# Kernel tuning notes

Measured on AMD Instinct MI355X. Metric: run time of the kernel, lower is better.

## Reference

```python
import jax, jax.numpy as jnp
import numpy as np

MARGIN = 0.3
NEG_FALLBACK = 1e6  # value used when a row has no negatives


def setup_inputs() -> dict:
    key = jax.random.key(0)
    k1, k2 = jax.random.split(key)
    N, D, NUM_IDS = 8192, 256, 512
    feat = jax.random.normal(k1, (N, D), dtype=jnp.float32)
    labels = jax.random.randint(k2, (N,), 0, NUM_IDS, dtype=jnp.int64)
    return {"feat": feat, "labels": labels}


def reference(feat, labels):
    N = feat.shape[0]
    sq_norms = jnp.sum(feat * feat, axis=1)  # [N]
    sq = sq_norms[:, None] + sq_norms[None, :] - 2.0 * (feat @ feat.T)  # [N,N]
    sq = jnp.maximum(sq, 0.0)
    # safe sqrt (zero distance on the diagonal would otherwise give nan grads)
    dist = jnp.where(sq > 0, jnp.sqrt(jnp.where(sq > 0, sq, 1.0)), 0.0)

    same = labels[:, None] == labels[None, :]          # [N,N] bool
    eye = jnp.eye(N, dtype=bool)
    is_pos = same & ~eye                                # exclude self-pair
    is_neg = ~same

    # hard mining: per-row masked max over positives / min over negatives
    dist_ap = jnp.where(is_pos.any(axis=1),
                        jnp.where(is_pos, dist, -jnp.inf).max(axis=1), 0.0)
    dist_an = jnp.where(is_neg.any(axis=1),
                        jnp.where(is_neg, dist, jnp.inf).min(axis=1), NEG_FALLBACK)

    # MarginRankingLoss with y=1: mean(relu(margin - (dist_an - dist_ap)))
    return jnp.mean(jnp.maximum(0.0, MARGIN + dist_ap - dist_an))
```

## Files before the change

### kernel.cpp

```cpp
#include <hip/hip_runtime.h>


constexpr int N = 8192;
constexpr int D = 256;
constexpr float MARGIN = 0.3f;
constexpr float NEG_FALLBACK = 1e6f;
constexpr float TBIG = 1e30f;

typedef __attribute__((ext_vector_type(8))) __bf16 bf16x8;
typedef __attribute__((ext_vector_type(4))) float f32x4;

__device__ __forceinline__ unsigned enc_f(float f) {
  unsigned u = __float_as_uint(f);
  return (u >> 31) ? ~u : (u | 0x80000000u);
}
__device__ __forceinline__ float dec_f(unsigned e) {
  unsigned u = (e >> 31) ? (e ^ 0x80000000u) : ~e;
  return __uint_as_float(u);
}
__device__ __forceinline__ unsigned short f2bf_rtn(float x) {
  unsigned u = __float_as_uint(x);
  return (unsigned short)((u + 0x7fffu + ((u >> 16) & 1u)) >> 16);
}


__global__ void tl_pass0f(const float* __restrict__ feat, float* __restrict__ norms,
                          unsigned* __restrict__ ap, unsigned* __restrict__ an,
                          unsigned short* __restrict__ P, float* __restrict__ out) {
  int row = blockIdx.x * 4 + (threadIdx.x >> 6);
  int lane = threadIdx.x & 63;
  float4 f = reinterpret_cast<const float4*>(feat + (size_t)row * D)[lane];
  ushort4 h;
  h.x = f2bf_rtn(f.x); h.y = f2bf_rtn(f.y); h.z = f2bf_rtn(f.z); h.w = f2bf_rtn(f.w);
  reinterpret_cast<ushort4*>(P + (size_t)row * D)[lane] = h;
  float s = fmaf(f.x, f.x, fmaf(f.y, f.y, fmaf(f.z, f.z, f.w * f.w)));
#pragma unroll
  for (int off = 32; off > 0; off >>= 1) s += __shfl_down(s, off, 64);
  if (lane == 0) {
    norms[row] = s;
    ap[row] = enc_f(-TBIG);
    an[row] = enc_f(TBIG);
  }
  if (row == 0 && lane == 0) out[0] = 0.0f;
}


__global__ __launch_bounds__(256, 3)
void tl_pass1m(const unsigned short* __restrict__ P, const int* __restrict__ labels,
               const float* __restrict__ norms,
               unsigned* __restrict__ ap, unsigned* __restrict__ an) {
  __shared__ unsigned short lbuf[2][128][64];

  unsigned short (*lA)[64] = lbuf[0];
  unsigned short (*lB)[64] = lbuf[1];

  const int tid = threadIdx.x;
  const int wave = tid >> 6;
  const int lane = tid & 63;
  const int c = lane & 15;
  const int q = lane >> 4;
  const int ib0 = blockIdx.y * 128;
  const int jb0 = blockIdx.x * 128;
  const int wi = (wave & 1) * 64;
  const int wj = (wave >> 1) * 64;

  f32x4 acc[4][4];
#pragma unroll
  for (int a = 0; a < 4; ++a)
#pragma unroll
    for (int b = 0; b < 4; ++b) acc[a][b] = (f32x4){0.f, 0.f, 0.f, 0.f};

  const int rsub = lane >> 3;
  const int gsw = (lane & 7) ^ (rsub & 7);

  for (int kc = 0; kc < D; kc += 64) {
#pragma unroll
    for (int t = 0; t < 4; ++t) {
      int rA = wave * 32 + t * 8;
      const unsigned short* gA = P + (size_t)(ib0 + rA + rsub) * D + kc + gsw * 8;
      __builtin_amdgcn_global_load_lds(
          (const __attribute__((address_space(1))) void*)gA,
          (__attribute__((address_space(3))) void*)&lA[rA][0], 16, 0, 0);
      const unsigned short* gB = P + (size_t)(jb0 + rA + rsub) * D + kc + gsw * 8;
      __builtin_amdgcn_global_load_lds(
          (const __attribute__((address_space(1))) void*)gB,
          (__attribute__((address_space(3))) void*)&lB[rA][0], 16, 0, 0);
    }
    __syncthreads();

#pragma unroll
    for (int ks = 0; ks < 2; ++ks) {
      bf16x8 af[4], bfr[4];
      const int gsel = ((ks * 4 + q) ^ (c & 7)) * 8;
#pragma unroll
      for (int a = 0; a < 4; ++a)
        af[a] = *(const bf16x8*)&lA[wi + a * 16 + c][gsel];
#pragma unroll
      for (int b = 0; b < 4; ++b)
        bfr[b] = *(const bf16x8*)&lB[wj + b * 16 + c][gsel];
#pragma unroll
      for (int a = 0; a < 4; ++a)
#pragma unroll
        for (int b = 0; b < 4; ++b)
          acc[a][b] = __builtin_amdgcn_mfma_f32_16x16x32_bf16(af[a], bfr[b], acc[a][b], 0, 0, 0);
    }
    __syncthreads();
  }

  int cj[4]; float nj[4]; int lj[4];
#pragma unroll
  for (int b = 0; b < 4; ++b) {
    cj[b] = jb0 + wj + b * 16 + c;
    nj[b] = norms[cj[b]];
    lj[b] = labels[cj[b]];
  }

  float tp[4][4], tn[4][4];
#pragma unroll
  for (int a = 0; a < 4; ++a) {
#pragma unroll
    for (int r = 0; r < 4; ++r) {
      int rg = ib0 + wi + a * 16 + q * 4 + r;
      int li = labels[rg];
      float vp = -TBIG, vn = TBIG;
#pragma unroll
      for (int b = 0; b < 4; ++b) {
        float t = fmaf(-2.f, acc[a][b][r], nj[b]);
        bool sm = (lj[b] == li);
        bool dg = (cj[b] == rg);
        vp = fmaxf(vp, (sm && !dg) ? t : -TBIG);
        vn = fminf(vn, sm ? TBIG : t);
      }
      tp[a][r] = vp;
      tn[a][r] = vn;
    }
  }

  float* S = (float*)lbuf;
  const int slot = (wave >> 1) * 16 + c;

#pragma unroll
  for (int a = 0; a < 4; ++a)
#pragma unroll
    for (int r = 0; r < 4; ++r)
      S[(wi + a * 16 + q * 4 + r) * 36 + slot] = tp[a][r];
  __syncthreads();
  float vp = 0.f;
  if (tid < 128) {
    const f32x4* Srow = (const f32x4*)&S[tid * 36];
    f32x4 m0 = Srow[0];
#pragma unroll
    for (int i = 1; i < 8; ++i) {
      f32x4 v = Srow[i];
      m0[0] = fmaxf(m0[0], v[0]); m0[1] = fmaxf(m0[1], v[1]);
      m0[2] = fmaxf(m0[2], v[2]); m0[3] = fmaxf(m0[3], v[3]);
    }
    vp = fmaxf(fmaxf(m0[0], m0[1]), fmaxf(m0[2], m0[3]));
  }
  __syncthreads();
#pragma unroll
  for (int a = 0; a < 4; ++a)
#pragma unroll
    for (int r = 0; r < 4; ++r)
      S[(wi + a * 16 + q * 4 + r) * 36 + slot] = tn[a][r];
  __syncthreads();
  if (tid < 128) {
    const f32x4* Srow = (const f32x4*)&S[tid * 36];
    f32x4 m0 = Srow[0];
#pragma unroll
    for (int i = 1; i < 8; ++i) {
      f32x4 v = Srow[i];
      m0[0] = fminf(m0[0], v[0]); m0[1] = fminf(m0[1], v[1]);
      m0[2] = fminf(m0[2], v[2]); m0[3] = fminf(m0[3], v[3]);
    }
    float vn = fminf(fminf(m0[0], m0[1]), fminf(m0[2], m0[3]));
    atomicMax(&ap[ib0 + tid], enc_f(vp));
    atomicMin(&an[ib0 + tid], enc_f(vn));
  }
}


__global__ void tl_pass2f(const unsigned* __restrict__ ap, const unsigned* __restrict__ an,
                          const float* __restrict__ norms, float* __restrict__ out) {
  int r = blockIdx.x * 256 + threadIdx.x;
  float ni = norms[r];
  float tpv = dec_f(ap[r]);
  float tnv = dec_f(an[r]);
  float dap = (tpv < -1e29f) ? 0.f : sqrtf(fmaxf(ni + tpv, 0.f));
  float dan = (tnv > 1e29f) ? NEG_FALLBACK : sqrtf(fmaxf(ni + tnv, 0.f));
  float v = fmaxf(0.f, MARGIN + dap - dan) * (1.0f / (float)N);
#pragma unroll
  for (int off = 32; off > 0; off >>= 1) v += __shfl_down(v, off, 64);
  __shared__ float red[4];
  int lane = threadIdx.x & 63, w = threadIdx.x >> 6;
  if (lane == 0) red[w] = v;
  __syncthreads();
  if (threadIdx.x == 0) atomicAdd(out, red[0] + red[1] + red[2] + red[3]);
}


constexpr int FB_BK = 32;
constexpr int FB_JSPLIT = 8;
constexpr int FB_JRANGE = N / FB_JSPLIT;
constexpr int FB_LDS = 132;

__global__ void tl_pass0_fb(const float* __restrict__ feat, float* __restrict__ norms,
                            float* __restrict__ ap, float* __restrict__ an,
                            float* __restrict__ out) {
  int row = blockIdx.x * 4 + (threadIdx.x >> 6);
  int lane = threadIdx.x & 63;
  float4 f = reinterpret_cast<const float4*>(feat + (size_t)row * D)[lane];
  float s = f.x * f.x + f.y * f.y + f.z * f.z + f.w * f.w;
#pragma unroll
  for (int off = 32; off > 0; off >>= 1) s += __shfl_down(s, off, 64);
  if (lane == 0) { norms[row] = s; ap[row] = 0.0f; an[row] = NEG_FALLBACK; }
  if (row == 0 && lane == 0) out[0] = 0.0f;
}

__global__ __launch_bounds__(256, 2)
void tl_pass1_fb(const float* __restrict__ feat, const int* __restrict__ labels,
                 const float* __restrict__ norms,
                 unsigned int* __restrict__ ap, unsigned int* __restrict__ an) {
  __shared__ float As[FB_BK][FB_LDS];
  __shared__ float Bs[FB_BK][FB_LDS];
  const int tid = threadIdx.x;
  const int tx = tid & 15, ty = tid >> 4;
  const int ib0 = blockIdx.y * 128;
  const int jbase = blockIdx.x * FB_JRANGE;
  float ni[8]; int li[8]; int ri[8];
#pragma unroll
  for (int a = 0; a < 8; ++a) {
    int r = ty * 4 + (a & 3) + ((a >> 2) << 6);
    ri[a] = ib0 + r; ni[a] = norms[ri[a]]; li[a] = labels[ri[a]];
  }
  float apv[8], anv[8];
#pragma unroll
  for (int a = 0; a < 8; ++a) { apv[a] = 0.0f; anv[a] = NEG_FALLBACK; }
  for (int jt = 0; jt < FB_JRANGE; jt += 128) {
    const int jb = jbase + jt;
    float acc[8][8];
#pragma unroll
    for (int a = 0; a < 8; ++a)
#pragma unroll
      for (int b = 0; b < 8; ++b) acc[a][b] = 0.0f;
    for (int kc = 0; kc < D; kc += FB_BK) {
#pragma unroll
      for (int u = 0; u < 4; ++u) {
        int lin = tid + u * 256;
        int row = lin >> 3, c4 = lin & 7;
        float4 va = *reinterpret_cast<const float4*>(feat + (size_t)(ib0 + row) * D + kc + c4 * 4);
        As[c4 * 4 + 0][row] = va.x; As[c4 * 4 + 1][row] = va.y;
        As[c4 * 4 + 2][row] = va.z; As[c4 * 4 + 3][row] = va.w;
        float4 vb = *reinterpret_cast<const float4*>(feat + (size_t)(jb + row) * D + kc + c4 * 4);
        Bs[c4 * 4 + 0][row] = vb.x; Bs[c4 * 4 + 1][row] = vb.y;
        Bs[c4 * 4 + 2][row] = vb.z; Bs[c4 * 4 + 3][row] = vb.w;
      }
      __syncthreads();
#pragma unroll 8
      for (int k = 0; k < FB_BK; ++k) {
        float4 a0 = *reinterpret_cast<const float4*>(&As[k][ty * 4]);
        float4 a1 = *reinterpret_cast<const float4*>(&As[k][64 + ty * 4]);
        float4 b0 = *reinterpret_cast<const float4*>(&Bs[k][tx * 4]);
        float4 b1 = *reinterpret_cast<const float4*>(&Bs[k][64 + tx * 4]);
        float av[8] = {a0.x, a0.y, a0.z, a0.w, a1.x, a1.y, a1.z, a1.w};
        float bv[8] = {b0.x, b0.y, b0.z, b0.w, b1.x, b1.y, b1.z, b1.w};
#pragma unroll
        for (int a = 0; a < 8; ++a)
#pragma unroll
          for (int b = 0; b < 8; ++b) acc[a][b] = fmaf(av[a], bv[b], acc[a][b]);
      }
      __syncthreads();
    }
#pragma unroll
    for (int b = 0; b < 8; ++b) {
      int cjx = jb + tx * 4 + (b & 3) + ((b >> 2) << 6);
      float njx = norms[cjx]; int ljx = labels[cjx];
#pragma unroll
      for (int a = 0; a < 8; ++a) {
        float sq = fmaxf(ni[a] + njx - 2.0f * acc[a][b], 0.0f);
        float dist = sqrtf(sq);
        if (li[a] == ljx) { if (ri[a] != cjx) apv[a] = fmaxf(apv[a], dist); }
        else anv[a] = fminf(anv[a], dist);
      }
    }
  }
  __syncthreads();
  float* red = &As[0][0];
#pragma unroll
  for (int a = 0; a < 8; ++a) {
    int r = ty * 4 + (a & 3) + ((a >> 2) << 6);
    red[r * 16 + tx] = apv[a];
  }
  __syncthreads();
  if (tid < 128) {
    float m = red[tid * 16];
#pragma unroll
    for (int t = 1; t < 16; ++t) m = fmaxf(m, red[tid * 16 + t]);
    atomicMax(&ap[ib0 + tid], __float_as_uint(m));
  }
  __syncthreads();
#pragma unroll
  for (int a = 0; a < 8; ++a) {
    int r = ty * 4 + (a & 3) + ((a >> 2) << 6);
    red[r * 16 + tx] = anv[a];
  }
  __syncthreads();
  if (tid < 128) {
    float m = red[tid * 16];
#pragma unroll
    for (int t = 1; t < 16; ++t) m = fminf(m, red[tid * 16 + t]);
    atomicMin(&an[ib0 + tid], __float_as_uint(m));
  }
}

__global__ void tl_pass2_fb(const float* __restrict__ ap, const float* __restrict__ an,
                            float* __restrict__ out) {
  int r = blockIdx.x * 256 + threadIdx.x;
  float v = fmaxf(0.0f, MARGIN + ap[r] - an[r]) * (1.0f / (float)N);
#pragma unroll
  for (int off = 32; off > 0; off >>= 1) v += __shfl_down(v, off, 64);
  __shared__ float red[4];
  int lane = threadIdx.x & 63, w = threadIdx.x >> 6;
  if (lane == 0) red[w] = v;
  __syncthreads();
  if (threadIdx.x == 0) atomicAdd(out, red[0] + red[1] + red[2] + red[3]);
}


extern "C" void kernel_launch(void* const* d_in, const int* in_sizes, int n_in,
                              void* d_out, int out_size, void* d_ws, size_t ws_size,
                              hipStream_t stream) {
  const float* feat = (const float*)d_in[0];
  const int* labels = (const int*)d_in[1];
  float* out = (float*)d_out;

  float* norms = (float*)d_ws;
  unsigned* ap = (unsigned*)(norms + N);
  unsigned* an = ap + N;
  unsigned short* P = (unsigned short*)(an + N + 4);
  const size_t NEED = 3 * (size_t)N * 4 + 16 + (size_t)N * D * 2;

  if (ws_size >= NEED) {
    tl_pass0f<<<N / 4, 256, 0, stream>>>(feat, norms, ap, an, P, out);
    dim3 grid1(N / 128, N / 128);
    tl_pass1m<<<grid1, 256, 0, stream>>>(P, labels, norms, ap, an);
    tl_pass2f<<<N / 256, 256, 0, stream>>>(ap, an, norms, out);
  } else {
    float* apf = (float*)ap;
    float* anf = (float*)an;
    tl_pass0_fb<<<N / 4, 256, 0, stream>>>(feat, norms, apf, anf, out);
    dim3 grid1(FB_JSPLIT, N / 128);
    tl_pass1_fb<<<grid1, 256, 0, stream>>>(feat, labels, norms, (unsigned*)apf, (unsigned*)anf);
    tl_pass2_fb<<<N / 256, 256, 0, stream>>>(apf, anf, out);
  }
}
```

Baseline: 110.5 us.

## Exploit Gram matrix symmetry to compute only upper-triangular tiles

Blocks below the diagonal now exit immediately. Each off-diagonal tile also reduces along columns, using the row norm, and updates the column rows' positive-max and negative-min via atomics. This roughly halves the MFMA work and global loads for the Gram matrix. In exchange it adds extra epilogue reductions, shared-memory traffic and atomics per tile, and leaves the grid imbalanced because half the blocks do nothing.

```diff
diff --git a/kernel.cpp b/kernel.cpp
--- a/kernel.cpp
+++ b/kernel.cpp
@@ -49,6 +49,8 @@
 void tl_pass1m(const unsigned short* __restrict__ P, const int* __restrict__ labels,
                const float* __restrict__ norms,
                unsigned* __restrict__ ap, unsigned* __restrict__ an) {
+  if (blockIdx.x < blockIdx.y) return;
+
   __shared__ unsigned short lbuf[2][128][64];
 
   unsigned short (*lA)[64] = lbuf[0];
@@ -61,6 +63,7 @@
   const int q = lane >> 4;
   const int ib0 = blockIdx.y * 128;
   const int jb0 = blockIdx.x * 128;
+  const bool offdiag = (ib0 != jb0);
   const int wi = (wave & 1) * 64;
   const int wj = (wave >> 1) * 64;
 
@@ -107,29 +110,40 @@
     __syncthreads();
   }
 
-  int cj[4]; float nj[4]; int lj[4];
+  int cj[4]; float njv[4]; int ljv[4];
 #pragma unroll
   for (int b = 0; b < 4; ++b) {
     cj[b] = jb0 + wj + b * 16 + c;
-    nj[b] = norms[cj[b]];
-    lj[b] = labels[cj[b]];
+    njv[b] = norms[cj[b]];
+    ljv[b] = labels[cj[b]];
   }
 
   float tp[4][4], tn[4][4];
+  float cp[4], cn[4];
+#pragma unroll
+  for (int b = 0; b < 4; ++b) { cp[b] = -TBIG; cn[b] = TBIG; }
+
 #pragma unroll
   for (int a = 0; a < 4; ++a) {
 #pragma unroll
     for (int r = 0; r < 4; ++r) {
       int rg = ib0 + wi + a * 16 + q * 4 + r;
       int li = labels[rg];
+      float ni = norms[rg];
       float vp = -TBIG, vn = TBIG;
 #pragma unroll
       for (int b = 0; b < 4; ++b) {
-        float t = fmaf(-2.f, acc[a][b][r], nj[b]);
-        bool sm = (lj[b] == li);
+        float dot = acc[a][b][r];
+        float t_r = fmaf(-2.f, dot, njv[b]);
+        bool sm = (ljv[b] == li);
         bool dg = (cj[b] == rg);
-        vp = fmaxf(vp, (sm && !dg) ? t : -TBIG);
-        vn = fminf(vn, sm ? TBIG : t);
+        vp = fmaxf(vp, (sm && !dg) ? t_r : -TBIG);
+        vn = fminf(vn, sm ? TBIG : t_r);
+        if (offdiag) {
+          float t_c = fmaf(-2.f, dot, ni);
+          cp[b] = fmaxf(cp[b], sm ? t_c : -TBIG);
+          cn[b] = fminf(cn[b], sm ? TBIG : t_c);
+        }
       }
       tp[a][r] = vp;
       tn[a][r] = vn;
@@ -176,6 +190,33 @@
     float vn = fminf(fminf(m0[0], m0[1]), fminf(m0[2], m0[3]));
     atomicMax(&ap[ib0 + tid], enc_f(vp));
     atomicMin(&an[ib0 + tid], enc_f(vn));
+  }
+
+  if (offdiag) {
+    __syncthreads();
+    float* S2p = (float*)lbuf;
+    float* S2n = S2p + 128 * 12;
+    const int slot2 = (wave & 1) * 4 + q;
+#pragma unroll
+    for (int b = 0; b < 4; ++b) {
+      S2p[(wj + b * 16 + c) * 12 + slot2] = cp[b];
+      S2n[(wj + b * 16 + c) * 12 + slot2] = cn[b];
+    }
+    __syncthreads();
+    if (tid < 128) {
+      const f32x4* Pr = (const f32x4*)&S2p[tid * 12];
+      f32x4 p0 = Pr[0], p1 = Pr[1];
+      p0[0] = fmaxf(p0[0], p1[0]); p0[1] = fmaxf(p0[1], p1[1]);
+      p0[2] = fmaxf(p0[2], p1[2]); p0[3] = fmaxf(p0[3], p1[3]);
+      float wp = fmaxf(fmaxf(p0[0], p0[1]), fmaxf(p0[2], p0[3]));
+      const f32x4* Nr = (const f32x4*)&S2n[tid * 12];
+      f32x4 n0 = Nr[0], n1 = Nr[1];
+      n0[0] = fminf(n0[0], n1[0]); n0[1] = fminf(n0[1], n1[1]);
+      n0[2] = fminf(n0[2], n1[2]); n0[3] = fminf(n0[3], n1[3]);
+      float wn = fminf(fminf(n0[0], n0[1]), fminf(n0[2], n0[3]));
+      atomicMax(&ap[jb0 + tid], enc_f(wp));
+      atomicMin(&an[jb0 + tid], enc_f(wn));
+    }
   }
 }
 
```

After: 115.2 us. 4.3% more time.

## Double-buffer LDS tiles in 32-wide K chunks to overlap loads with MFMA

Applied to the files above, without the earlier changes.

Splits the K loop of the distance GEMM into eight 32-wide chunks and ping-pongs between two LDS buffers. The next chunk is prefetched with global_load_lds while MFMAs run on the current one. The loop now has one barrier per chunk, and the shared-memory swizzle pattern changes to suit the narrower rows. The aim is to hide global-to-LDS latency behind compute. In exchange there are more, smaller loop iterations and a new bank-conflict pattern.

```diff
diff --git a/kernel.cpp b/kernel.cpp
--- a/kernel.cpp
+++ b/kernel.cpp
@@ -49,10 +49,7 @@
 void tl_pass1m(const unsigned short* __restrict__ P, const int* __restrict__ labels,
                const float* __restrict__ norms,
                unsigned* __restrict__ ap, unsigned* __restrict__ an) {
-  __shared__ unsigned short lbuf[2][128][64];
-
-  unsigned short (*lA)[64] = lbuf[0];
-  unsigned short (*lB)[64] = lbuf[1];
+  __shared__ unsigned short lbuf[2][2][128][32];
 
   const int tid = threadIdx.x;
   const int wave = tid >> 6;
@@ -70,42 +67,51 @@
 #pragma unroll
     for (int b = 0; b < 4; ++b) acc[a][b] = (f32x4){0.f, 0.f, 0.f, 0.f};
 
-  const int rsub = lane >> 3;
-  const int gsw = (lane & 7) ^ (rsub & 7);
-
-  for (int kc = 0; kc < D; kc += 64) {
-#pragma unroll
-    for (int t = 0; t < 4; ++t) {
-      int rA = wave * 32 + t * 8;
-      const unsigned short* gA = P + (size_t)(ib0 + rA + rsub) * D + kc + gsw * 8;
-      __builtin_amdgcn_global_load_lds(
-          (const __attribute__((address_space(1))) void*)gA,
-          (__attribute__((address_space(3))) void*)&lA[rA][0], 16, 0, 0);
-      const unsigned short* gB = P + (size_t)(jb0 + rA + rsub) * D + kc + gsw * 8;
-      __builtin_amdgcn_global_load_lds(
-          (const __attribute__((address_space(1))) void*)gB,
-          (__attribute__((address_space(3))) void*)&lB[rA][0], 16, 0, 0);
-    }
+  const int srow = lane >> 2;
+  const int sg = ((lane & 3) - (lane >> 3)) & 3;
+  const int slot = ((q + (c >> 1)) & 3) * 8;
+
+#define STAGE(ck, bb)                                                          \
+  {                                                                            \
+    _Pragma("unroll")                                                          \
+    for (int t = 0; t < 4; ++t) {                                              \
+      int idx = wave * 4 + t;             \
+      int m = idx >> 3;                                                        \
+      int rb = (idx & 7) * 16;                                                 \
+      int base = m ? jb0 : ib0;                                                \
+      const unsigned short* gp =                                               \
+          P + (size_t)(base + rb + srow) * D + (ck) * 32 + sg * 8;             \
+      __builtin_amdgcn_global_load_lds(                                        \
+          (const __attribute__((address_space(1))) void*)gp,                   \
+          (__attribute__((address_space(3))) void*)&lbuf[bb][m][rb][0],        \
+          16, 0, 0);                                                           \
+    }                                                                          \
+  }
+
+  STAGE(0, 0);
+  __syncthreads();
+
+#pragma unroll
+  for (int ck = 0; ck < 8; ++ck) {
+    const int bb = ck & 1;
+    if (ck < 7) STAGE(ck + 1, bb ^ 1);
+
+    bf16x8 af[4], bfr[4];
+#pragma unroll
+    for (int a = 0; a < 4; ++a)
+      af[a] = *(const bf16x8*)&lbuf[bb][0][wi + a * 16 + c][slot];
+#pragma unroll
+    for (int b = 0; b < 4; ++b)
+      bfr[b] = *(const bf16x8*)&lbuf[bb][1][wj + b * 16 + c][slot];
+#pragma unroll
+    for (int a = 0; a < 4; ++a)
+#pragma unroll
+      for (int b = 0; b < 4; ++b)
+        acc[a][b] = __builtin_amdgcn_mfma_f32_16x16x32_bf16(af[a], bfr[b], acc[a][b], 0, 0, 0);
+
     __syncthreads();
-
-#pragma unroll
-    for (int ks = 0; ks < 2; ++ks) {
-      bf16x8 af[4], bfr[4];
-      const int gsel = ((ks * 4 + q) ^ (c & 7)) * 8;
-#pragma unroll
-      for (int a = 0; a < 4; ++a)
-        af[a] = *(const bf16x8*)&lA[wi + a * 16 + c][gsel];
-#pragma unroll
-      for (int b = 0; b < 4; ++b)
-        bfr[b] = *(const bf16x8*)&lB[wj + b * 16 + c][gsel];
-#pragma unroll
-      for (int a = 0; a < 4; ++a)
-#pragma unroll
-        for (int b = 0; b < 4; ++b)
-          acc[a][b] = __builtin_amdgcn_mfma_f32_16x16x32_bf16(af[a], bfr[b], acc[a][b], 0, 0, 0);
-    }
-    __syncthreads();
-  }
+  }
+#undef STAGE
 
   int cj[4]; float nj[4]; int lj[4];
 #pragma unroll
@@ -137,13 +143,13 @@
   }
 
   float* S = (float*)lbuf;
-  const int slot = (wave >> 1) * 16 + c;
+  const int slot2 = (wave >> 1) * 16 + c;
 
 #pragma unroll
   for (int a = 0; a < 4; ++a)
 #pragma unroll
     for (int r = 0; r < 4; ++r)
-      S[(wi + a * 16 + q * 4 + r) * 36 + slot] = tp[a][r];
+      S[(wi + a * 16 + q * 4 + r) * 36 + slot2] = tp[a][r];
   __syncthreads();
   float vp = 0.f;
   if (tid < 128) {
@@ -162,7 +168,7 @@
   for (int a = 0; a < 4; ++a)
 #pragma unroll
     for (int r = 0; r < 4; ++r)
-      S[(wi + a * 16 + q * 4 + r) * 36 + slot] = tn[a][r];
+      S[(wi + a * 16 + q * 4 + r) * 36 + slot2] = tn[a][r];
   __syncthreads();
   if (tid < 128) {
     const f32x4* Srow = (const f32x4*)&S[tid * 36];
```

Result: slower. 122.8 us (+11.1%).
